# Optimization experiments

Measured on AMD Instinct MI355X. Metric: run time of the kernel, lower is better.

The kernel has to match this reference:

```python
import jax, jax.numpy as jnp
import numpy as np

N_NODES = 100000
N_EDGES = 1000000
D_IN = 64
D_MODEL = 64  # H * D
H = 4
D = D_MODEL // H


def setup_inputs() -> dict:
    key = jax.random.key(0)
    ks = jax.random.split(key, 9)
    nodes = jax.random.normal(ks[0], (N_NODES, D_IN), dtype=jnp.float32)
    senders = jax.random.randint(ks[1], (N_EDGES,), 0, N_NODES, dtype=jnp.int32)
    receivers = jnp.sort(jax.random.randint(ks[2], (N_EDGES,), 0, N_NODES, dtype=jnp.int32))
    s = 1.0 / np.sqrt(D_IN)
    W_qk = jax.random.uniform(ks[3], (D_IN, D_MODEL), jnp.float32, -s, s)
    b_qk = jnp.zeros((D_MODEL,), jnp.float32)
    W_v = jax.random.uniform(ks[4], (D_IN, D_MODEL), jnp.float32, -s, s)
    b_v = jnp.zeros((D_MODEL,), jnp.float32)
    so = 1.0 / np.sqrt(D_MODEL)
    W_out = jax.random.uniform(ks[5], (D_MODEL, D_MODEL), jnp.float32, -so, so)
    b_out = jnp.zeros((D_MODEL,), jnp.float32)
    return {
        'nodes': nodes, 'W_qk': W_qk, 'b_qk': b_qk, 'W_v': W_v, 'b_v': b_v,
        'W_out': W_out, 'b_out': b_out, 'senders': senders, 'receivers': receivers,
    }


def _segment_softmax(logits, segment_ids, num_segments):
    # jraph-style numerically stable segment softmax (segments are sorted)
    maxs = jax.ops.segment_max(logits, segment_ids, num_segments, indices_are_sorted=True)
    e = jnp.exp(logits - maxs[segment_ids])
    z = jax.ops.segment_sum(e, segment_ids, num_segments, indices_are_sorted=True)
    return e / z[segment_ids]


def reference(nodes, W_qk, b_qk, W_v, b_v, W_out, b_out, senders, receivers):
    N = nodes.shape[0]
    # projections: N (H D) -> N H D
    qks = (nodes @ W_qk + b_qk).reshape(N, H, D)
    vs = (nodes @ W_v + b_v).reshape(N, H, D)
    # per-edge QK scores: [E, H]
    scores = jnp.einsum('ehd,ehd->eh', qks[receivers], qks[senders])
    attn = _segment_softmax(scores, receivers, N)
    # weighted message scatter: [E,H,D] -> [N, H*D]
    messages = (attn[..., None] * vs[senders]).reshape(-1, H * D)
    ctx = jax.ops.segment_sum(messages, receivers, N, indices_are_sorted=True)
    out = ctx @ W_out + b_out
    return out, attn
```

## Files before the change

kernel.cpp:

```cpp
#include <hip/hip_runtime.h>
#include <math.h>


typedef _Float16 h2 __attribute__((ext_vector_type(2)));
typedef _Float16 half8 __attribute__((ext_vector_type(8)));
typedef float floatx4 __attribute__((ext_vector_type(4)));

#define WT_PAD 72

__global__ __launch_bounds__(256) void mhga_proj_rowptr(
    const float* __restrict__ X,
    const float* __restrict__ Wqk, const float* __restrict__ bqk,
    const float* __restrict__ Wv,  const float* __restrict__ bv,
    unsigned char* __restrict__ packed,
    const int* __restrict__ receivers, int* __restrict__ row_ptr,
    int N, int E, int PB)
{
    if ((int)blockIdx.x >= PB) {
        const int n = (blockIdx.x - PB) * 256 + threadIdx.x;
        if (n > N) return;
        int lo = 0, hi = E;
        while (lo < hi) {
            const int mid = (lo + hi) >> 1;
            if (receivers[mid] < n) lo = mid + 1; else hi = mid;
        }
        row_ptr[n] = lo;
        return;
    }

    __shared__ __align__(16) _Float16 Xh[64 * WT_PAD];
    __shared__ __align__(16) _Float16 Wt[128 * WT_PAD];
    const int t = threadIdx.x;
    const int m0 = blockIdx.x * 64;

#pragma unroll
    for (int rep = 0; rep < 4; ++rep) {
        const int idx = t * 4 + rep * 1024;
        const int m = idx >> 6, k = idx & 63;
        float4 xv = make_float4(0.f, 0.f, 0.f, 0.f);
        if (m0 + m < N) xv = *(const float4*)(X + (size_t)(m0 + m) * 64 + k);
        h2 lo = { (_Float16)xv.x, (_Float16)xv.y };
        h2 hi = { (_Float16)xv.z, (_Float16)xv.w };
        uint2 u = make_uint2(__builtin_bit_cast(unsigned, lo),
                             __builtin_bit_cast(unsigned, hi));
        *(uint2*)(&Xh[m * WT_PAD + k]) = u;
    }
#pragma unroll
    for (int rep = 0; rep < 8; ++rep) {
        const int idx = t * 4 + rep * 1024;
        const int k = idx >> 7, j = idx & 127;
        const float4 wv = (j < 64) ? *(const float4*)(Wqk + k * 64 + j)
                                   : *(const float4*)(Wv + k * 64 + (j - 64));
        const float w4[4] = {wv.x, wv.y, wv.z, wv.w};
#pragma unroll
        for (int i = 0; i < 4; ++i) {
            const int n = j + i;
            Wt[n * WT_PAD + (k ^ ((n & 7) * 8))] = (_Float16)w4[i];
        }
    }
    __syncthreads();

    const int w = t >> 6, lane = t & 63;
    const int ln = lane & 15, quad = lane >> 4;

    const half8 a0 = *(const half8*)(&Xh[(w * 16 + ln) * WT_PAD + quad * 8]);
    const half8 a1 = *(const half8*)(&Xh[(w * 16 + ln) * WT_PAD + 32 + quad * 8]);

    float bt[8];
#pragma unroll
    for (int tt = 0; tt < 8; ++tt)
        bt[tt] = (tt < 4) ? bqk[tt * 16 + ln] : bv[(tt - 4) * 16 + ln];

    floatx4 acc[8];
#pragma unroll
    for (int tt = 0; tt < 8; ++tt) {
        const int n = tt * 16 + ln;
        const int swz = (n & 7);
        const half8 b0 = *(const half8*)(&Wt[n * WT_PAD + ((quad ^ swz) * 8)]);
        const half8 b1 = *(const half8*)(&Wt[n * WT_PAD + (((4 + quad) ^ swz) * 8)]);
        floatx4 c = {0.f, 0.f, 0.f, 0.f};
        c = __builtin_amdgcn_mfma_f32_16x16x32_f16(a0, b0, c, 0, 0, 0);
        c = __builtin_amdgcn_mfma_f32_16x16x32_f16(a1, b1, c, 0, 0, 0);
        acc[tt] = c;
    }

#pragma unroll
    for (int tt = 0; tt < 8; ++tt) {
        const int off = (tt < 4)
            ? ((tt * 4 + (ln >> 2)) * 16 + (ln & 3) * 2)
            : (((tt - 4) * 4 + (ln >> 2)) * 16 + 8 + (ln & 3) * 2);
#pragma unroll
        for (int r = 0; r < 4; ++r) {
            const int row = m0 + w * 16 + quad * 4 + r;
            if (row < N)
                *(_Float16*)(packed + (size_t)row * 256 + off) =
                    (_Float16)(acc[tt][r] + bt[tt]);
        }
    }
}

__global__ __launch_bounds__(256) void mhga_attn(
    const unsigned char* __restrict__ packed,
    const int* __restrict__ senders, const int* __restrict__ row_ptr,
    const float* __restrict__ Wout, const float* __restrict__ bout,
    float* __restrict__ p_ws, float* __restrict__ out,
    float* __restrict__ attn_out, int N)
{
    __shared__ float sW[64 * 64];
    __shared__ float sCtx[4][64];
    const int t = threadIdx.x;
#pragma unroll
    for (int i = t * 4; i < 4096; i += 1024)
        *(float4*)(sW + i) = *(const float4*)(Wout + i);

    const int wave = t >> 6, lane = t & 63;
    const int g = lane >> 4, tl = lane & 15;
    const float bo = bout[lane];
    __syncthreads();

    for (int n = blockIdx.x * 4 + wave; n < N; n += gridDim.x * 4) {
        const int e0 = row_ptr[n];
        const int e1 = row_ptr[n + 1];
        float l = 0.f;
        float4 ctx = make_float4(0.f, 0.f, 0.f, 0.f);
        const uint4 qpk = *(const uint4*)(packed + (size_t)n * 256 + tl * 16);
        const h2 q0 = __builtin_bit_cast(h2, qpk.x);
        const h2 q1 = __builtin_bit_cast(h2, qpk.y);

        for (int base = e0; base < e1; base += 64) {
            const int cnt = min(64, e1 - base);
            int sid = 0;
            if (base + lane < e1) sid = senders[base + lane];
            const int iters = (cnt + 3) >> 2;
            for (int i = 0; i < iters; ++i) {
                const int idx = i * 4 + g;
                const int s = __shfl(sid, idx, 64);
                if (idx < cnt) {
                    const uint4 pk =
                        *(const uint4*)(packed + (size_t)s * 256 + tl * 16);
                    const h2 k0 = __builtin_bit_cast(h2, pk.x);
                    const h2 k1 = __builtin_bit_cast(h2, pk.y);
                    const h2 v0 = __builtin_bit_cast(h2, pk.z);
                    const h2 v1 = __builtin_bit_cast(h2, pk.w);
                    float d = __builtin_amdgcn_fdot2(q0, k0, 0.f, false);
                    d = __builtin_amdgcn_fdot2(q1, k1, d, false);
                    d += __shfl_xor(d, 1, 64);
                    d += __shfl_xor(d, 2, 64);
                    const float p = __expf(d);
                    if ((tl & 3) == 0)
                        p_ws[(size_t)(base + idx) * 4 + (tl >> 2)] = p;
                    l += p;
                    ctx.x = fmaf(p, (float)v0.x, ctx.x);
                    ctx.y = fmaf(p, (float)v0.y, ctx.y);
                    ctx.z = fmaf(p, (float)v1.x, ctx.z);
                    ctx.w = fmaf(p, (float)v1.y, ctx.w);
                }
            }
        }
#pragma unroll
        for (int mask = 16; mask <= 32; mask <<= 1) {
            l     += __shfl_xor(l, mask, 64);
            ctx.x += __shfl_xor(ctx.x, mask, 64);
            ctx.y += __shfl_xor(ctx.y, mask, 64);
            ctx.z += __shfl_xor(ctx.z, mask, 64);
            ctx.w += __shfl_xor(ctx.w, mask, 64);
        }
        const float inv = (l > 0.f) ? (1.f / l) : 0.f;
        if (g == 0) {
            *(float4*)(&sCtx[wave][tl * 4]) =
                make_float4(ctx.x * inv, ctx.y * inv, ctx.z * inv, ctx.w * inv);
        }

        __builtin_amdgcn_s_waitcnt(0x0F70);

        const float lh = __shfl(l, (lane & 3) << 2, 64);
        const float invl = (lh > 0.f) ? (1.f / lh) : 0.f;
        volatile const float* vp = p_ws;
        for (int f = e0 * 4 + lane; f < e1 * 4; f += 64)
            attn_out[f] = vp[f] * invl;

        float acc = bo;
#pragma unroll
        for (int k = 0; k < 64; k += 4) {
            const float4 c = *(const float4*)(&sCtx[wave][k]);
            acc = fmaf(c.x, sW[(k + 0) * 64 + lane], acc);
            acc = fmaf(c.y, sW[(k + 1) * 64 + lane], acc);
            acc = fmaf(c.z, sW[(k + 2) * 64 + lane], acc);
            acc = fmaf(c.w, sW[(k + 3) * 64 + lane], acc);
        }
        out[(size_t)n * 64 + lane] = acc;
    }
}

extern "C" void kernel_launch(void* const* d_in, const int* in_sizes, int n_in,
                              void* d_out, int out_size, void* d_ws, size_t ws_size,
                              hipStream_t stream) {
    const float* nodes   = (const float*)d_in[0];
    const float* W_qk    = (const float*)d_in[1];
    const float* b_qk    = (const float*)d_in[2];
    const float* W_v     = (const float*)d_in[3];
    const float* b_v     = (const float*)d_in[4];
    const float* W_out   = (const float*)d_in[5];
    const float* b_out   = (const float*)d_in[6];
    const int* senders   = (const int*)d_in[7];
    const int* receivers = (const int*)d_in[8];

    const int N = in_sizes[0] / 64;
    const int E = in_sizes[7];

    float* out      = (float*)d_out;
    float* attn_out = out + (size_t)N * 64;

    unsigned char* packed = (unsigned char*)d_ws;
    int*   rowp = (int*)(packed + (size_t)N * 256);
    float* p_ws = (float*)(rowp + (((N + 1) + 3) & ~3));

    const int PB = (N + 63) / 64;
    const int RB = (N + 1 + 255) / 256;
    mhga_proj_rowptr<<<PB + RB, 256, 0, stream>>>(
        nodes, W_qk, b_qk, W_v, b_v, packed, receivers, rowp, N, E, PB);

    mhga_attn<<<2048, 256, 0, stream>>>(packed, senders, rowp,
                                        W_out, b_out, p_ws, out, attn_out, N);
}
```

Measured before the change: 198.7 us.

## Split weight prep into separate kernel and stage projection output through LDS

The weight transpose and fp16 conversion move into a small prep kernel that also computes row pointers and writes a transposed fp16 weight matrix to workspace. The projection kernel now reads X and the weights straight from global memory into MFMA operands with no LDS staging or barrier. Its output goes into an LDS tile and is written back with coalesced 16-byte stores instead of scattered 2-byte stores. This adds a third kernel launch and extra workspace, and every block now re-reads the weights from global or L2.

```diff
diff --git a/kernel.cpp b/kernel.cpp
--- a/kernel.cpp
+++ b/kernel.cpp
@@ -6,78 +6,61 @@
 typedef _Float16 half8 __attribute__((ext_vector_type(8)));
 typedef float floatx4 __attribute__((ext_vector_type(4)));
 
-#define WT_PAD 72
-
-__global__ __launch_bounds__(256) void mhga_proj_rowptr(
-    const float* __restrict__ X,
-    const float* __restrict__ Wqk, const float* __restrict__ bqk,
-    const float* __restrict__ Wv,  const float* __restrict__ bv,
-    unsigned char* __restrict__ packed,
+#define SP_ROW 136
+
+__global__ __launch_bounds__(256) void mhga_prep(
+    const float* __restrict__ Wqk, const float* __restrict__ Wv,
+    _Float16* __restrict__ Wt,
     const int* __restrict__ receivers, int* __restrict__ row_ptr,
-    int N, int E, int PB)
+    int N, int E)
 {
-    if ((int)blockIdx.x >= PB) {
-        const int n = (blockIdx.x - PB) * 256 + threadIdx.x;
-        if (n > N) return;
-        int lo = 0, hi = E;
-        while (lo < hi) {
-            const int mid = (lo + hi) >> 1;
-            if (receivers[mid] < n) lo = mid + 1; else hi = mid;
-        }
-        row_ptr[n] = lo;
+    if ((int)blockIdx.x < 32) {
+        const int idx = blockIdx.x * 256 + threadIdx.x;
+        const int n = idx >> 6, k = idx & 63;
+        const float w = (n < 64) ? Wqk[k * 64 + n] : Wv[k * 64 + (n - 64)];
+        Wt[idx] = (_Float16)w;
         return;
     }
-
-    __shared__ __align__(16) _Float16 Xh[64 * WT_PAD];
-    __shared__ __align__(16) _Float16 Wt[128 * WT_PAD];
+    const int n = (blockIdx.x - 32) * 256 + threadIdx.x;
+    if (n > N) return;
+    int lo = 0, hi = E;
+    while (lo < hi) {
+        const int mid = (lo + hi) >> 1;
+        if (receivers[mid] < n) lo = mid + 1; else hi = mid;
+    }
+    row_ptr[n] = lo;
+}
+
+__global__ __launch_bounds__(256) void mhga_proj(
+    const float* __restrict__ X, const _Float16* __restrict__ Wt,
+    const float* __restrict__ bqk, const float* __restrict__ bv,
+    unsigned char* __restrict__ packed, int N)
+{
+    __shared__ __align__(16) _Float16 sP[64 * SP_ROW];
     const int t = threadIdx.x;
-    const int m0 = blockIdx.x * 64;
-
-#pragma unroll
-    for (int rep = 0; rep < 4; ++rep) {
-        const int idx = t * 4 + rep * 1024;
-        const int m = idx >> 6, k = idx & 63;
-        float4 xv = make_float4(0.f, 0.f, 0.f, 0.f);
-        if (m0 + m < N) xv = *(const float4*)(X + (size_t)(m0 + m) * 64 + k);
-        h2 lo = { (_Float16)xv.x, (_Float16)xv.y };
-        h2 hi = { (_Float16)xv.z, (_Float16)xv.w };
-        uint2 u = make_uint2(__builtin_bit_cast(unsigned, lo),
-                             __builtin_bit_cast(unsigned, hi));
-        *(uint2*)(&Xh[m * WT_PAD + k]) = u;
-    }
-#pragma unroll
-    for (int rep = 0; rep < 8; ++rep) {
-        const int idx = t * 4 + rep * 1024;
-        const int k = idx >> 7, j = idx & 127;
-        const float4 wv = (j < 64) ? *(const float4*)(Wqk + k * 64 + j)
-                                   : *(const float4*)(Wv + k * 64 + (j - 64));
-        const float w4[4] = {wv.x, wv.y, wv.z, wv.w};
-#pragma unroll
-        for (int i = 0; i < 4; ++i) {
-            const int n = j + i;
-            Wt[n * WT_PAD + (k ^ ((n & 7) * 8))] = (_Float16)w4[i];
-        }
-    }
-    __syncthreads();
-
     const int w = t >> 6, lane = t & 63;
     const int ln = lane & 15, quad = lane >> 4;
-
-    const half8 a0 = *(const half8*)(&Xh[(w * 16 + ln) * WT_PAD + quad * 8]);
-    const half8 a1 = *(const half8*)(&Xh[(w * 16 + ln) * WT_PAD + 32 + quad * 8]);
-
-    float bt[8];
-#pragma unroll
-    for (int tt = 0; tt < 8; ++tt)
-        bt[tt] = (tt < 4) ? bqk[tt * 16 + ln] : bv[(tt - 4) * 16 + ln];
+    const int m0 = blockIdx.x * 64;
+
+    const int arow = min(m0 + w * 16 + ln, N - 1);
+    const float* xr = X + (size_t)arow * 64;
+    const float4 xa = *(const float4*)(xr + quad * 8);
+    const float4 xb = *(const float4*)(xr + quad * 8 + 4);
+    const float4 xc = *(const float4*)(xr + 32 + quad * 8);
+    const float4 xd = *(const float4*)(xr + 32 + quad * 8 + 4);
+    const half8 a0 = { (_Float16)xa.x, (_Float16)xa.y, (_Float16)xa.z,
+                       (_Float16)xa.w, (_Float16)xb.x, (_Float16)xb.y,
+                       (_Float16)xb.z, (_Float16)xb.w };
+    const half8 a1 = { (_Float16)xc.x, (_Float16)xc.y, (_Float16)xc.z,
+                       (_Float16)xc.w, (_Float16)xd.x, (_Float16)xd.y,
+                       (_Float16)xd.z, (_Float16)xd.w };
 
     floatx4 acc[8];
 #pragma unroll
     for (int tt = 0; tt < 8; ++tt) {
-        const int n = tt * 16 + ln;
-        const int swz = (n & 7);
-        const half8 b0 = *(const half8*)(&Wt[n * WT_PAD + ((quad ^ swz) * 8)]);
-        const half8 b1 = *(const half8*)(&Wt[n * WT_PAD + (((4 + quad) ^ swz) * 8)]);
+        const _Float16* wrow = Wt + (tt * 16 + ln) * 64;
+        const half8 b0 = *(const half8*)(wrow + quad * 8);
+        const half8 b1 = *(const half8*)(wrow + 32 + quad * 8);
         floatx4 c = {0.f, 0.f, 0.f, 0.f};
         c = __builtin_amdgcn_mfma_f32_16x16x32_f16(a0, b0, c, 0, 0, 0);
         c = __builtin_amdgcn_mfma_f32_16x16x32_f16(a1, b1, c, 0, 0, 0);
@@ -86,16 +69,24 @@
 
 #pragma unroll
     for (int tt = 0; tt < 8; ++tt) {
-        const int off = (tt < 4)
-            ? ((tt * 4 + (ln >> 2)) * 16 + (ln & 3) * 2)
-            : (((tt - 4) * 4 + (ln >> 2)) * 16 + 8 + (ln & 3) * 2);
+        const float bt = (tt < 4) ? bqk[tt * 16 + ln] : bv[(tt - 4) * 16 + ln];
+        const int j = (tt & 3) * 16 + ln;
+        const int fidx = (j >> 2) * 8 + ((tt < 4) ? 0 : 4) + (j & 3);
 #pragma unroll
         for (int r = 0; r < 4; ++r) {
-            const int row = m0 + w * 16 + quad * 4 + r;
-            if (row < N)
-                *(_Float16*)(packed + (size_t)row * 256 + off) =
-                    (_Float16)(acc[tt][r] + bt[tt]);
-        }
+            const int lrow = w * 16 + quad * 4 + r;
+            sP[lrow * SP_ROW + fidx] = (_Float16)(acc[tt][r] + bt);
+        }
+    }
+
+    const int crow = w * 16 + (lane >> 2);
+    const int grow = m0 + crow;
+    if (grow < N) {
+        const _Float16* src = sP + crow * SP_ROW + (lane & 3) * 32;
+        unsigned char* dst = packed + (size_t)grow * 256 + (lane & 3) * 64;
+#pragma unroll
+        for (int c = 0; c < 4; ++c)
+            *(uint4*)(dst + c * 16) = *(const uint4*)(src + c * 8);
     }
 }
 
@@ -214,12 +205,12 @@
     unsigned char* packed = (unsigned char*)d_ws;
     int*   rowp = (int*)(packed + (size_t)N * 256);
     float* p_ws = (float*)(rowp + (((N + 1) + 3) & ~3));
-
-    const int PB = (N + 63) / 64;
+    _Float16* Wt = (_Float16*)(p_ws + (size_t)E * 4);
+
     const int RB = (N + 1 + 255) / 256;
-    mhga_proj_rowptr<<<PB + RB, 256, 0, stream>>>(
-        nodes, W_qk, b_qk, W_v, b_v, packed, receivers, rowp, N, E, PB);
-
+    mhga_prep<<<32 + RB, 256, 0, stream>>>(W_qk, W_v, Wt, receivers, rowp, N, E);
+    mhga_proj<<<(N + 63) / 64, 256, 0, stream>>>(nodes, Wt, b_qk, b_v,
+                                                 packed, N);
     mhga_attn<<<2048, 256, 0, stream>>>(packed, senders, rowp,
                                         W_out, b_out, p_ws, out, attn_out, N);
 }
```

New measurement: 191.7 us. 1.04x faster.
